# Optimization experiments

Measured on AMD Instinct MI355X. Metric: run time of the kernel, lower is better.

Reference implementation:

```python
import jax, jax.numpy as jnp
import numpy as np
import math

B, T, HID = 2, 2048, 2048
NH, KVH, HD = 16, 4, 128  # num_heads, kv_heads, head_dim


def rotate_half(x):
    x1, x2 = x[..., : x.shape[-1] // 2], x[..., x.shape[-1] // 2 :]
    return jnp.concatenate([-x2, x1], axis=-1)


def setup_inputs() -> dict:
    key = jax.random.key(0)
    ks = jax.random.split(key, 6)
    hidden_states = jax.random.normal(ks[0], (B, T, HID), dtype=jnp.float32)
    # additive causal mask (0 on/below diag, -inf-ish above)
    causal = jnp.triu(jnp.full((T, T), -1e9, dtype=jnp.float32), k=1)
    attention_mask = causal[None, None, :, :]
    # real RoPE angles
    inv_freq = 1.0 / (10000.0 ** (np.arange(0, HD, 2, dtype=np.float32) / HD))
    t = np.arange(T, dtype=np.float32)
    freqs = np.einsum('t,d->td', t, inv_freq)
    emb = np.concatenate([freqs, freqs], axis=-1)  # (T, HD)
    cos = jnp.asarray(np.cos(emb))[None, None, :, :]
    sin = jnp.asarray(np.sin(emb))[None, None, :, :]
    s = 0.02
    Wq = jax.random.normal(ks[1], (HID, NH * HD), dtype=jnp.float32) * s
    Wk = jax.random.normal(ks[2], (HID, KVH * HD), dtype=jnp.float32) * s
    Wv = jax.random.normal(ks[3], (HID, KVH * HD), dtype=jnp.float32) * s
    Wo = jax.random.normal(ks[4], (HID, HID), dtype=jnp.float32) * s
    return dict(hidden_states=hidden_states, attention_mask=attention_mask,
                cos=cos, sin=sin, Wq=Wq, Wk=Wk, Wv=Wv, Wo=Wo)


def reference(hidden_states, attention_mask, cos, sin, Wq, Wk, Wv, Wo):
    b, t, _ = hidden_states.shape
    # projections; weights stored (in, out) so y = x @ W
    q = (hidden_states @ Wq).reshape(b, t, NH, HD).transpose(0, 2, 1, 3)   # (B,H,T,D)
    k = (hidden_states @ Wk).reshape(b, t, KVH, HD).transpose(0, 2, 1, 3)  # (B,Hkv,T,D)
    v = (hidden_states @ Wv).reshape(b, t, KVH, HD).transpose(0, 2, 1, 3)
    # RoPE
    c, s = cos[:, :, :t, :], sin[:, :, :t, :]
    q = q * c + rotate_half(q) * s
    k = k * c + rotate_half(k) * s
    # GQA: repeat_interleave kv heads
    rf = NH // KVH
    k = jnp.repeat(k, rf, axis=1)
    v = jnp.repeat(v, rf, axis=1)
    scores = jnp.einsum('bhtd,bhsd->bhts', q, k) / math.sqrt(HD)
    scores = scores + attention_mask
    probs = jax.nn.softmax(scores.astype(jnp.float32), axis=-1).astype(q.dtype)
    ctx = jnp.einsum('bhts,bhsd->bhtd', probs, v)
    ctx = ctx.transpose(0, 2, 1, 3).reshape(b, t, HID)
    return ctx @ Wo
```

## Files before the change

kernel.cpp:

```cpp
#include <hip/hip_runtime.h>
#include <hip/hip_bf16.h>
#include <math.h>

typedef __bf16 bf16;
typedef __bf16 bf16x4 __attribute__((ext_vector_type(4)));
typedef __bf16 bf16x8 __attribute__((ext_vector_type(8)));
typedef float f32x4 __attribute__((ext_vector_type(4)));

#define B_   2
#define T_   2048
#define HID_ 2048
#define NH_  16
#define KVH_ 4
#define HD_  128

__device__ __forceinline__ void gload_lds16(const bf16* g, bf16* l) {
    __builtin_amdgcn_global_load_lds(
        (const __attribute__((address_space(1))) unsigned int*)g,
        (__attribute__((address_space(3))) unsigned int*)l, 16, 0, 0);
}

__device__ __forceinline__ bf16x8 cat4(bf16x4 a, bf16x4 b) {
    bf16x8 r;
    #pragma unroll
    for (int i = 0; i < 4; i++) { r[i] = a[i]; r[i + 4] = b[i]; }
    return r;
}

__device__ __forceinline__ void transpose_tile(const float* __restrict__ in, bf16* __restrict__ out,
                                               int N, int rowOff, int kt, int nt) {
    __shared__ float tile[32][33];
    int k0 = kt * 32, n0 = nt * 32;
    int tx = threadIdx.x & 31, ty = threadIdx.x >> 5;
    for (int i = ty; i < 32; i += 8)
        tile[i][tx] = in[(size_t)(k0 + i) * N + n0 + tx];
    __syncthreads();
    for (int i = ty; i < 32; i += 8)
        out[(size_t)(rowOff + n0 + i) * 2048 + (k0 + tx)] = (bf16)tile[tx][i];
}

__global__ void prep(const float* __restrict__ hidden, bf16* __restrict__ hid_bf,
                     const float* __restrict__ Wq, const float* __restrict__ Wk,
                     const float* __restrict__ Wv, const float* __restrict__ Wo,
                     bf16* __restrict__ WqkvT, bf16* __restrict__ WoT) {
    int bid = blockIdx.x;
    if (bid < 8192) {
        int i = bid * 256 + threadIdx.x;
        float4 v = ((const float4*)hidden)[i];
        bf16x4 o = { (bf16)v.x, (bf16)v.y, (bf16)v.z, (bf16)v.w };
        ((bf16x4*)hid_bf)[i] = o;
    } else if (bid < 12288) {
        int t = bid - 8192;
        transpose_tile(Wq, WqkvT, 2048, 0, t & 63, t >> 6);
    } else if (bid < 13312) {
        int t = bid - 12288;
        transpose_tile(Wk, WqkvT, 512, 2048, t & 63, t >> 6);
    } else if (bid < 14336) {
        int t = bid - 13312;
        transpose_tile(Wv, WqkvT, 512, 2560, t & 63, t >> 6);
    } else {
        int t = bid - 14336;
        transpose_tile(Wo, WoT, 2048, 0, t & 63, t >> 6);
    }
}


__global__ __launch_bounds__(256, 2) void gemm_qkv_rope(
    const bf16* __restrict__ A, const bf16* __restrict__ BT,
    const float* __restrict__ cosb, const float* __restrict__ sinb,
    bf16* __restrict__ q, bf16* __restrict__ k, bf16* __restrict__ vT) {
    __shared__ __align__(16) char smem[128 * 136 * 2];
    bf16* As = (bf16*)smem;
    bf16* Bs = As + 128 * 32;
    bf16* Cs = (bf16*)smem;
    const int K = 2048;
    int bm = blockIdx.x * 128, hid = blockIdx.y, bn = hid * 128;
    int tid = threadIdx.x, lane = tid & 63, w = tid >> 6;
    int wm = (w & 1) * 64, wn = (w >> 1) * 64;
    int lm = lane & 15, quad = lane >> 4;
    int c0 = w * 64 + lane, c1 = 256 + c0;
    int r0 = c0 >> 2, g0 = (((c0 & 3) ^ ((c0 >> 3) & 3)) * 8);
    int r1 = c1 >> 2, g1 = (((c1 & 3) ^ ((c1 >> 3) & 3)) * 8);
    const bf16* a0 = A  + (size_t)(bm + r0) * K + g0;
    const bf16* a1 = A  + (size_t)(bm + r1) * K + g1;
    const bf16* b0 = BT + (size_t)(bn + r0) * K + g0;
    const bf16* b1 = BT + (size_t)(bn + r1) * K + g1;
    bf16* lA0 = As + (size_t)(w * 64) * 8;
    bf16* lA1 = As + (size_t)(256 + w * 64) * 8;
    bf16* lB0 = Bs + (size_t)(w * 64) * 8;
    bf16* lB1 = Bs + (size_t)(256 + w * 64) * 8;
    int sx = ((quad ^ ((lm >> 1) & 3)) << 3);
    f32x4 acc[4][4] = {};
    for (int k0 = 0; k0 < K; k0 += 32) {
        gload_lds16(a0, lA0); gload_lds16(a1, lA1);
        gload_lds16(b0, lB0); gload_lds16(b1, lB1);
        a0 += 32; a1 += 32; b0 += 32; b1 += 32;
        __syncthreads();
        bf16x8 af[4], bfr[4];
        #pragma unroll
        for (int mt = 0; mt < 4; mt++) af[mt]  = *(const bf16x8*)&As[(wm + mt*16 + lm) * 32 + sx];
        #pragma unroll
        for (int nt = 0; nt < 4; nt++) bfr[nt] = *(const bf16x8*)&Bs[(wn + nt*16 + lm) * 32 + sx];
        #pragma unroll
        for (int mt = 0; mt < 4; mt++)
            #pragma unroll
            for (int nt = 0; nt < 4; nt++)
                acc[mt][nt] = __builtin_amdgcn_mfma_f32_16x16x32_bf16(af[mt], bfr[nt], acc[mt][nt], 0, 0, 0);
        __syncthreads();
    }
    #pragma unroll
    for (int mt = 0; mt < 4; mt++)
        #pragma unroll
        for (int r = 0; r < 4; r++) {
            int row = wm + mt*16 + quad*4 + r;
            #pragma unroll
            for (int nt = 0; nt < 4; nt++)
                Cs[row * 136 + wn + nt*16 + lm] = (bf16)acc[mt][nt][r];
        }
    __syncthreads();

    int b = bm >> 11, t0 = bm & 2047;
    if (hid < 20) {
        bool isq = hid < 16;
        int d = (tid & 15) * 8;
        float sgn = (d < 64) ? -1.f : 1.f;
        float scl = isq ? 0.12752965013239224f : 1.0f;
        bf16* dst = isq ? (q + ((size_t)(b * NH_ + hid) * T_) * HD_)
                        : (k + ((size_t)(b * KVH_ + (hid - 16)) * T_) * HD_);
        #pragma unroll
        for (int i = 0; i < 8; i++) {
            int row = (tid >> 4) + i * 16;
            int t = t0 + row;
            bf16x8 x  = *(const bf16x8*)&Cs[row * 136 + d];
            bf16x8 xo = *(const bf16x8*)&Cs[row * 136 + (d ^ 64)];
            bf16x8 o;
            #pragma unroll
            for (int j = 0; j < 8; j++) {
                float c = cosb[t * 128 + d + j], s = sinb[t * 128 + d + j];
                o[j] = (bf16)(((float)x[j] * c + sgn * (float)xo[j] * s) * scl);
            }
            *(bf16x8*)(dst + (size_t)t * HD_ + d) = o;
        }
    } else {
        int kvh = hid - 20;
        int t6 = (tid & 15) * 4;
        int C = 4 * (t6 >> 5) + ((t6 >> 2) & 3);
        int j0 = 4 * ((t6 >> 4) & 1);
        int pos = 8 * C + j0;
        bf16* dst = vT + (size_t)(b * KVH_ + kvh) * HD_ * T_;
        #pragma unroll
        for (int i = 0; i < 8; i++) {
            int d = (tid >> 4) + i * 16;
            #pragma unroll
            for (int half = 0; half < 2; half++) {
                int tt = half * 64 + t6;
                bf16x4 vv = { Cs[(tt+0)*136 + d], Cs[(tt+1)*136 + d],
                              Cs[(tt+2)*136 + d], Cs[(tt+3)*136 + d] };
                *(bf16x4*)(dst + (size_t)d * T_ + t0 + half * 64 + pos) = vv;
            }
        }
    }
}

__global__ __launch_bounds__(256, 2) void gemm_bf16_nt(
    const bf16* __restrict__ A, const bf16* __restrict__ BT, float* __restrict__ C,
    int M, int N, int K) {
    __shared__ __align__(16) bf16 As[128 * 32];
    __shared__ __align__(16) bf16 Bs[128 * 32];
    int bm = blockIdx.x * 128, bn = blockIdx.y * 128;
    int tid = threadIdx.x, lane = tid & 63, w = tid >> 6;
    int wm = (w & 1) * 64, wn = (w >> 1) * 64;
    int lm = lane & 15, quad = lane >> 4;
    int c0 = w * 64 + lane, c1 = 256 + c0;
    int r0 = c0 >> 2, g0 = (((c0 & 3) ^ ((c0 >> 3) & 3)) * 8);
    int r1 = c1 >> 2, g1 = (((c1 & 3) ^ ((c1 >> 3) & 3)) * 8);
    const bf16* a0 = A  + (size_t)(bm + r0) * K + g0;
    const bf16* a1 = A  + (size_t)(bm + r1) * K + g1;
    const bf16* b0 = BT + (size_t)(bn + r0) * K + g0;
    const bf16* b1 = BT + (size_t)(bn + r1) * K + g1;
    bf16* lA0 = As + (size_t)(w * 64) * 8;
    bf16* lA1 = As + (size_t)(256 + w * 64) * 8;
    bf16* lB0 = Bs + (size_t)(w * 64) * 8;
    bf16* lB1 = Bs + (size_t)(256 + w * 64) * 8;
    int sx = ((quad ^ ((lm >> 1) & 3)) << 3);
    f32x4 acc[4][4] = {};
    for (int k0 = 0; k0 < K; k0 += 32) {
        gload_lds16(a0, lA0); gload_lds16(a1, lA1);
        gload_lds16(b0, lB0); gload_lds16(b1, lB1);
        a0 += 32; a1 += 32; b0 += 32; b1 += 32;
        __syncthreads();
        bf16x8 af[4], bfr[4];
        #pragma unroll
        for (int mt = 0; mt < 4; mt++) af[mt]  = *(const bf16x8*)&As[(wm + mt*16 + lm) * 32 + sx];
        #pragma unroll
        for (int nt = 0; nt < 4; nt++) bfr[nt] = *(const bf16x8*)&Bs[(wn + nt*16 + lm) * 32 + sx];
        #pragma unroll
        for (int mt = 0; mt < 4; mt++)
            #pragma unroll
            for (int nt = 0; nt < 4; nt++)
                acc[mt][nt] = __builtin_amdgcn_mfma_f32_16x16x32_bf16(af[mt], bfr[nt], acc[mt][nt], 0, 0, 0);
        __syncthreads();
    }
    #pragma unroll
    for (int mt = 0; mt < 4; mt++) {
        #pragma unroll
        for (int r = 0; r < 4; r++) {
            int row = bm + wm + mt*16 + quad*4 + r;
            float* cp = C + (size_t)row * N + bn + wn + lm;
            #pragma unroll
            for (int nt = 0; nt < 4; nt++)
                cp[nt*16] = acc[mt][nt][r];
        }
    }
}

__global__ __launch_bounds__(256, 2) void flash_attn(
    const bf16* __restrict__ q, const bf16* __restrict__ k, const bf16* __restrict__ vT,
    bf16* __restrict__ ctx) {
    __shared__ __align__(16) bf16 Ksb[2 * 64 * 128];
    __shared__ __align__(16) bf16 Vpb[2 * 128 * 64];
    int bh = blockIdx.y;
    int b = bh >> 4, h = bh & 15, kvh = h >> 2;
    int tid = threadIdx.x, lane = tid & 63, w = tid >> 6;
    int lm = lane & 15, quad = lane >> 4, kq = quad * 8;
    const bf16* kg = k  + (size_t)(b * KVH_ + kvh) * T_ * HD_;
    const bf16* vg = vT + (size_t)(b * KVH_ + kvh) * HD_ * T_;
    int ksl = lane >> 4;
    int vdl = lane >> 3;
    int vc  = (((lane & 7) ^ (vdl & 7)) << 3);
    int sxv1 = ((quad ^ (lm & 7)) << 3);
    int sxv2 = (((4 + quad) ^ (lm & 7)) << 3);

    auto stage = [&](int s0, int p) {
        bf16* kd = Ksb + p * (64 * 128);
        bf16* vd = Vpb + p * (128 * 64);
        #pragma unroll
        for (int i = 0; i < 4; i++) {
            int srow = w * 16 + i * 4;
            int kc = (((lane & 15) ^ (i * 4 + ksl)) << 3);
            gload_lds16(kg + (size_t)(s0 + srow + ksl) * HD_ + kc, kd + srow * 128);
        }
        #pragma unroll
        for (int i = 0; i < 4; i++) {
            int drow = w * 32 + i * 8;
            gload_lds16(vg + (size_t)(drow + vdl) * T_ + s0 + vc, vd + drow * 64);
        }
    };

    for (int half = 0; half < 2; half++) {
        int qt = (half == 0) ? blockIdx.x : (31 - blockIdx.x);
        const bf16* qg = q + ((size_t)(b * NH_ + h) * T_ + qt*64 + w*16 + lm) * HD_;
        bf16x8 qf[4];
        #pragma unroll
        for (int kk = 0; kk < 4; kk++) qf[kk] = *(const bf16x8*)(qg + kk*32 + kq);

        f32x4 Ot[8] = {};
        float l_ = 0.f;
        int nIter = qt + 1;

        __syncthreads();
        stage(0, 0);

        for (int it = 0; it < nIter; it++) {
            __syncthreads();
            if (it + 1 < nIter) stage((it + 1) * 64, (it + 1) & 1);
            const bf16* ks = Ksb + (it & 1) * (64 * 128);
            const bf16* vp = Vpb + (it & 1) * (128 * 64);

            f32x4 sacc[4] = {};
            #pragma unroll
            for (int n = 0; n < 4; n++)
                #pragma unroll
                for (int kk = 0; kk < 4; kk++) {
                    bf16x8 kf = *(const bf16x8*)&ks[(n*16 + lm) * 128 + (((kk*4 + quad) ^ lm) << 3)];
                    sacc[n] = __builtin_amdgcn_mfma_f32_16x16x32_bf16(kf, qf[kk], sacc[n], 0, 0, 0);
                }
            if (it == qt) {
                #pragma unroll
                for (int n = 0; n < 4; n++)
                    #pragma unroll
                    for (int r = 0; r < 4; r++)
                        if (n*16 + quad*4 + r > w*16 + lm) sacc[n][r] = -1e30f;
            }
            bf16x4 pt[4];
            #pragma unroll
            for (int n = 0; n < 4; n++) {
                f32x4 pe;
                #pragma unroll
                for (int r = 0; r < 4; r++) pe[r] = exp2f(sacc[n][r]);
                l_ += (pe[0] + pe[1]) + (pe[2] + pe[3]);
                #pragma unroll
                for (int r = 0; r < 4; r++) pt[n][r] = (bf16)pe[r];
            }
            bf16x8 pf01 = cat4(pt[0], pt[1]);
            bf16x8 pf23 = cat4(pt[2], pt[3]);
            #pragma unroll
            for (int dt = 0; dt < 8; dt++) {
                const bf16* vr = &vp[(dt*16 + lm) * 64];
                bf16x8 vf01 = *(const bf16x8*)(vr + sxv1);
                Ot[dt] = __builtin_amdgcn_mfma_f32_16x16x32_bf16(vf01, pf01, Ot[dt], 0, 0, 0);
                bf16x8 vf23 = *(const bf16x8*)(vr + sxv2);
                Ot[dt] = __builtin_amdgcn_mfma_f32_16x16x32_bf16(vf23, pf23, Ot[dt], 0, 0, 0);
            }
        }

        l_ += __shfl_xor(l_, 16);
        l_ += __shfl_xor(l_, 32);
        float linv = 1.0f / l_;
        bf16* cp = ctx + ((size_t)(b * T_) + qt*64 + w*16 + lm) * HID_ + h * HD_;
        #pragma unroll
        for (int dt = 0; dt < 8; dt++) {
            bf16x4 o4 = { (bf16)(Ot[dt][0]*linv), (bf16)(Ot[dt][1]*linv),
                          (bf16)(Ot[dt][2]*linv), (bf16)(Ot[dt][3]*linv) };
            *(bf16x4*)(cp + dt*16 + quad*4) = o4;
        }
    }
}

extern "C" void kernel_launch(void* const* d_in, const int* in_sizes, int n_in,
                              void* d_out, int out_size, void* d_ws, size_t ws_size,
                              hipStream_t stream) {
    const float* hidden = (const float*)d_in[0];
    const float* cosb = (const float*)d_in[2];
    const float* sinb = (const float*)d_in[3];
    const float* Wq = (const float*)d_in[4];
    const float* Wk = (const float*)d_in[5];
    const float* Wv = (const float*)d_in[6];
    const float* Wo = (const float*)d_in[7];
    float* out = (float*)d_out;

    char* ws = (char*)d_ws;
    size_t off = 0;
    bf16* hid_bf = (bf16*)(ws + off); off += (size_t)4096*2048*2;
    bf16* WqkvT  = (bf16*)(ws + off); off += (size_t)3072*2048*2;
    bf16* WoT    = (bf16*)(ws + off); off += (size_t)2048*2048*2;
    bf16* qbuf   = (bf16*)(ws + off); off += (size_t)B_*NH_*T_*HD_*2;
    bf16* kbuf   = (bf16*)(ws + off); off += (size_t)B_*KVH_*T_*HD_*2;
    bf16* vtbuf  = (bf16*)(ws + off); off += (size_t)B_*KVH_*HD_*T_*2;
    bf16* ctx    = (bf16*)(ws + off); off += (size_t)4096*2048*2;

    prep<<<18432, 256, 0, stream>>>(hidden, hid_bf, Wq, Wk, Wv, Wo, WqkvT, WoT);
    gemm_qkv_rope<<<dim3(32, 24), 256, 0, stream>>>(hid_bf, WqkvT, cosb, sinb, qbuf, kbuf, vtbuf);
    flash_attn<<<dim3(16, 32), 256, 0, stream>>>(qbuf, kbuf, vtbuf, ctx);
    gemm_bf16_nt<<<dim3(32, 16), 256, 0, stream>>>(ctx, WoT, out, 4096, 2048, 2048);
}
```

Baseline: 299.3 us.

## Rewrite QKV GEMM as 256x256 double-buffered pipelined tile with 8 waves

The QKV projection GEMM moves from 128x128 tiles with a single LDS buffer and BK=32 to 256x256 tiles, 512 threads, BK=64 and a double-buffered LDS ring. Global-to-LDS loads for the next K step are issued between MFMA phases, with s_setprio raised around the MFMA groups, so that memory latency overlaps compute. The RoPE/V-transpose epilogue now processes two heads per block in two passes through a 128-row-stride staging area. The larger tile improves data reuse but uses 128KB of LDS, which limits residency, and leaves only 192 blocks for the GPU's 256 CUs.

```diff
diff --git a/kernel.cpp b/kernel.cpp
--- a/kernel.cpp
+++ b/kernel.cpp
@@ -64,99 +64,189 @@
     }
 }
 
-
-__global__ __launch_bounds__(256, 2) void gemm_qkv_rope(
+__global__ __launch_bounds__(512, 2) void gemm_qkv_rope(
     const bf16* __restrict__ A, const bf16* __restrict__ BT,
     const float* __restrict__ cosb, const float* __restrict__ sinb,
     bf16* __restrict__ q, bf16* __restrict__ k, bf16* __restrict__ vT) {
-    __shared__ __align__(16) char smem[128 * 136 * 2];
-    bf16* As = (bf16*)smem;
-    bf16* Bs = As + 128 * 32;
-    bf16* Cs = (bf16*)smem;
+    __shared__ __align__(16) bf16 smem[2 * 32768];
+    bf16* Cs = smem;
     const int K = 2048;
-    int bm = blockIdx.x * 128, hid = blockIdx.y, bn = hid * 128;
+    int bm = blockIdx.x * 256, by = blockIdx.y, bn = by * 256;
     int tid = threadIdx.x, lane = tid & 63, w = tid >> 6;
-    int wm = (w & 1) * 64, wn = (w >> 1) * 64;
+    int wcol = w & 3;
+    int wm = (w >> 2) * 128, wn = wcol * 64;
     int lm = lane & 15, quad = lane >> 4;
-    int c0 = w * 64 + lane, c1 = 256 + c0;
-    int r0 = c0 >> 2, g0 = (((c0 & 3) ^ ((c0 >> 3) & 3)) * 8);
-    int r1 = c1 >> 2, g1 = (((c1 & 3) ^ ((c1 >> 3) & 3)) * 8);
-    const bf16* a0 = A  + (size_t)(bm + r0) * K + g0;
-    const bf16* a1 = A  + (size_t)(bm + r1) * K + g1;
-    const bf16* b0 = BT + (size_t)(bn + r0) * K + g0;
-    const bf16* b1 = BT + (size_t)(bn + r1) * K + g1;
-    bf16* lA0 = As + (size_t)(w * 64) * 8;
-    bf16* lA1 = As + (size_t)(256 + w * 64) * 8;
-    bf16* lB0 = Bs + (size_t)(w * 64) * 8;
-    bf16* lB1 = Bs + (size_t)(256 + w * 64) * 8;
-    int sx = ((quad ^ ((lm >> 1) & 3)) << 3);
-    f32x4 acc[4][4] = {};
-    for (int k0 = 0; k0 < K; k0 += 32) {
-        gload_lds16(a0, lA0); gload_lds16(a1, lA1);
-        gload_lds16(b0, lB0); gload_lds16(b1, lB1);
-        a0 += 32; a1 += 32; b0 += 32; b1 += 32;
+    int srow = tid >> 3;
+    int scol = ((tid & 7) * 8) ^ ((srow & 7) << 3);
+    const bf16* ga = A  + (size_t)(bm + srow) * K + scol;
+    const bf16* gb = BT + (size_t)(bn + srow) * K + scol;
+    int ldst = w * 512;
+    int fxo = (lm & 7) << 3;
+    f32x4 acc[8][4] = {};
+    bf16x8 af[4][2], b0[2][2], b1[2][2];
+
+#define BARx() do { asm volatile("" ::: "memory");                              \
+                    __builtin_amdgcn_s_barrier();                               \
+                    asm volatile("" ::: "memory"); } while (0)
+
+#define RD_A(MH, CB) do {                                                       \
+        _Pragma("unroll")                                                       \
+        for (int mf = 0; mf < 4; ++mf)                                          \
+            _Pragma("unroll")                                                   \
+            for (int ks = 0; ks < 2; ++ks)                                      \
+                af[mf][ks] = *(const bf16x8*)&(CB)[(wm + (MH)*64 + mf*16 + lm)*64 \
+                                                   + ((ks*32 + quad*8) ^ fxo)]; \
+    } while (0)
+
+#define RD_B(DST, NH, CB) do {                                                  \
+        _Pragma("unroll")                                                       \
+        for (int nf = 0; nf < 2; ++nf)                                          \
+            _Pragma("unroll")                                                   \
+            for (int ks = 0; ks < 2; ++ks)                                      \
+                DST[nf][ks] = *(const bf16x8*)&(CB)[16384                       \
+                                    + (wn + ((NH)*2 + nf)*16 + lm)*64           \
+                                    + ((ks*32 + quad*8) ^ fxo)];                \
+    } while (0)
+
+#define MM(MH, NH, BF) do {                                                     \
+        __builtin_amdgcn_s_setprio(1);                                          \
+        _Pragma("unroll")                                                       \
+        for (int mf = 0; mf < 4; ++mf)                                          \
+            _Pragma("unroll")                                                   \
+            for (int nf = 0; nf < 2; ++nf)                                      \
+                _Pragma("unroll")                                               \
+                for (int ks = 0; ks < 2; ++ks)                                  \
+                    acc[(MH)*4 + mf][(NH)*2 + nf] =                             \
+                        __builtin_amdgcn_mfma_f32_16x16x32_bf16(                \
+                            af[mf][ks], BF[nf][ks],                             \
+                            acc[(MH)*4 + mf][(NH)*2 + nf], 0, 0, 0);            \
+        __builtin_amdgcn_s_setprio(0);                                          \
+    } while (0)
+
+#define STAGE_H(H, NB) do {                                                     \
+        _Pragma("unroll")                                                       \
+        for (int j = 0; j < 2; ++j) {                                           \
+            gload_lds16(ga + 64 + (size_t)((H)*128 + j*64) * K,                 \
+                        (NB) + (H)*8192 + j*4096 + ldst);                       \
+            gload_lds16(gb + 64 + (size_t)((H)*128 + j*64) * K,                 \
+                        (NB) + 16384 + (H)*8192 + j*4096 + ldst);               \
+        }                                                                       \
+    } while (0)
+
+    #pragma unroll
+    for (int h = 0; h < 2; ++h)
+        #pragma unroll
+        for (int j = 0; j < 2; ++j) {
+            gload_lds16(ga + (size_t)(h*128 + j*64) * K, smem + h*8192 + j*4096 + ldst);
+            gload_lds16(gb + (size_t)(h*128 + j*64) * K, smem + 16384 + h*8192 + j*4096 + ldst);
+        }
+    asm volatile("s_waitcnt vmcnt(0)" ::: "memory");
+    BARx();
+
+    for (int t = 0; t < 31; ++t) {
+        bf16* cb = smem + (t & 1) * 32768;
+        bf16* nb = smem + ((t + 1) & 1) * 32768;
+        RD_A(0, cb);
+        RD_B(b0, 0, cb);
+        STAGE_H(0, nb);
+        BARx();
+        MM(0, 0, b0);
+        asm volatile("s_waitcnt vmcnt(4)" ::: "memory");
+        BARx();
+        RD_B(b1, 1, cb);
+        STAGE_H(1, nb);
+        BARx();
+        MM(0, 1, b1);
+        BARx();
+        RD_A(1, cb);
+        BARx();
+        MM(1, 1, b1);
+        BARx();
+        MM(1, 0, b0);
+        asm volatile("s_waitcnt vmcnt(4)" ::: "memory");
+        BARx();
+        ga += 64; gb += 64;
+    }
+    {
+        bf16* cb = smem + 32768;
+        RD_A(0, cb);
+        RD_B(b0, 0, cb);
+        BARx();
+        MM(0, 0, b0);
+        asm volatile("s_waitcnt vmcnt(0)" ::: "memory");
+        BARx();
+        RD_B(b1, 1, cb);
+        BARx();
+        MM(0, 1, b1);
+        BARx();
+        RD_A(1, cb);
+        BARx();
+        MM(1, 1, b1);
+        BARx();
+        MM(1, 0, b0);
+        BARx();
+    }
+#undef BARx
+#undef RD_A
+#undef RD_B
+#undef MM
+#undef STAGE_H
+
+    int b = bm >> 11, t0 = bm & 2047;
+    for (int hh = 0; hh < 2; ++hh) {
         __syncthreads();
-        bf16x8 af[4], bfr[4];
-        #pragma unroll
-        for (int mt = 0; mt < 4; mt++) af[mt]  = *(const bf16x8*)&As[(wm + mt*16 + lm) * 32 + sx];
-        #pragma unroll
-        for (int nt = 0; nt < 4; nt++) bfr[nt] = *(const bf16x8*)&Bs[(wn + nt*16 + lm) * 32 + sx];
-        #pragma unroll
-        for (int mt = 0; mt < 4; mt++)
-            #pragma unroll
-            for (int nt = 0; nt < 4; nt++)
-                acc[mt][nt] = __builtin_amdgcn_mfma_f32_16x16x32_bf16(af[mt], bfr[nt], acc[mt][nt], 0, 0, 0);
+        if ((wcol >> 1) == hh) {
+            #pragma unroll
+            for (int mfg = 0; mfg < 8; ++mfg)
+                #pragma unroll
+                for (int r = 0; r < 4; ++r) {
+                    int row = wm + (mfg >> 2) * 64 + (mfg & 3) * 16 + quad * 4 + r;
+                    #pragma unroll
+                    for (int nfg = 0; nfg < 4; ++nfg)
+                        Cs[row * 136 + (wcol & 1) * 64 + nfg * 16 + lm] = (bf16)acc[mfg][nfg][r];
+                }
+        }
         __syncthreads();
-    }
-    #pragma unroll
-    for (int mt = 0; mt < 4; mt++)
-        #pragma unroll
-        for (int r = 0; r < 4; r++) {
-            int row = wm + mt*16 + quad*4 + r;
-            #pragma unroll
-            for (int nt = 0; nt < 4; nt++)
-                Cs[row * 136 + wn + nt*16 + lm] = (bf16)acc[mt][nt][r];
-        }
-    __syncthreads();
-
-    int b = bm >> 11, t0 = bm & 2047;
-    if (hid < 20) {
-        bool isq = hid < 16;
-        int d = (tid & 15) * 8;
-        float sgn = (d < 64) ? -1.f : 1.f;
-        float scl = isq ? 0.12752965013239224f : 1.0f;
-        bf16* dst = isq ? (q + ((size_t)(b * NH_ + hid) * T_) * HD_)
-                        : (k + ((size_t)(b * KVH_ + (hid - 16)) * T_) * HD_);
-        #pragma unroll
-        for (int i = 0; i < 8; i++) {
-            int row = (tid >> 4) + i * 16;
-            int t = t0 + row;
-            bf16x8 x  = *(const bf16x8*)&Cs[row * 136 + d];
-            bf16x8 xo = *(const bf16x8*)&Cs[row * 136 + (d ^ 64)];
-            bf16x8 o;
-            #pragma unroll
-            for (int j = 0; j < 8; j++) {
-                float c = cosb[t * 128 + d + j], s = sinb[t * 128 + d + j];
-                o[j] = (bf16)(((float)x[j] * c + sgn * (float)xo[j] * s) * scl);
+        if (by < 10) {
+            bool isq = by < 8;
+            int hd = isq ? (by * 2 + hh) : ((by - 8) * 2 + hh);
+            int d = (tid & 15) * 8;
+            float sgn = (d < 64) ? -1.f : 1.f;
+            float scl = isq ? 0.12752965013239224f : 1.0f;
+            bf16* dst = isq ? (q + ((size_t)(b * NH_ + hd) * T_) * HD_)
+                            : (k + ((size_t)(b * KVH_ + hd) * T_) * HD_);
+            #pragma unroll
+            for (int i = 0; i < 8; ++i) {
+                int row = (tid >> 4) + i * 32;
+                int t = t0 + row;
+                bf16x8 x  = *(const bf16x8*)&Cs[row * 136 + d];
+                bf16x8 xo = *(const bf16x8*)&Cs[row * 136 + (d ^ 64)];
+                bf16x8 o;
+                #pragma unroll
+                for (int j = 0; j < 8; ++j) {
+                    float c = cosb[t * 128 + d + j], s = sinb[t * 128 + d + j];
+                    o[j] = (bf16)(((float)x[j] * c + sgn * (float)xo[j] * s) * scl);
+                }
+                *(bf16x8*)(dst + (size_t)t * HD_ + d) = o;
             }
-            *(bf16x8*)(dst + (size_t)t * HD_ + d) = o;
-        }
-    } else {
-        int kvh = hid - 20;
-        int t6 = (tid & 15) * 4;
-        int C = 4 * (t6 >> 5) + ((t6 >> 2) & 3);
-        int j0 = 4 * ((t6 >> 4) & 1);
-        int pos = 8 * C + j0;
-        bf16* dst = vT + (size_t)(b * KVH_ + kvh) * HD_ * T_;
-        #pragma unroll
-        for (int i = 0; i < 8; i++) {
-            int d = (tid >> 4) + i * 16;
-            #pragma unroll
-            for (int half = 0; half < 2; half++) {
-                int tt = half * 64 + t6;
-                bf16x4 vv = { Cs[(tt+0)*136 + d], Cs[(tt+1)*136 + d],
-                              Cs[(tt+2)*136 + d], Cs[(tt+3)*136 + d] };
-                *(bf16x4*)(dst + (size_t)d * T_ + t0 + half * 64 + pos) = vv;
+        } else {
+            int kvh = (by - 10) * 2 + hh;
+            int tb = tid >> 8, tl = tid & 255;
+            int t6 = (tl & 15) * 4;
+            int Cc = 4 * (t6 >> 5) + ((t6 >> 2) & 3);
+            int j0 = 4 * ((t6 >> 4) & 1);
+            int pos = 8 * Cc + j0;
+            bf16* dst = vT + (size_t)(b * KVH_ + kvh) * HD_ * T_;
+            #pragma unroll
+            for (int i = 0; i < 8; ++i) {
+                int d = (tl >> 4) + i * 16;
+                #pragma unroll
+                for (int hv = 0; hv < 2; ++hv) {
+                    int rr = tb * 128 + hv * 64 + t6;
+                    bf16x4 vv = { Cs[(rr + 0) * 136 + d], Cs[(rr + 1) * 136 + d],
+                                  Cs[(rr + 2) * 136 + d], Cs[(rr + 3) * 136 + d] };
+                    *(bf16x4*)(dst + (size_t)d * T_ + t0 + tb * 128 + hv * 64 + pos) = vv;
+                }
             }
         }
     }
@@ -340,7 +430,7 @@
     bf16* ctx    = (bf16*)(ws + off); off += (size_t)4096*2048*2;
 
     prep<<<18432, 256, 0, stream>>>(hidden, hid_bf, Wq, Wk, Wv, Wo, WqkvT, WoT);
-    gemm_qkv_rope<<<dim3(32, 24), 256, 0, stream>>>(hid_bf, WqkvT, cosb, sinb, qbuf, kbuf, vtbuf);
+    gemm_qkv_rope<<<dim3(16, 12), 512, 0, stream>>>(hid_bf, WqkvT, cosb, sinb, qbuf, kbuf, vtbuf);
     flash_attn<<<dim3(16, 32), 256, 0, stream>>>(qbuf, kbuf, vtbuf, ctx);
     gemm_bf16_nt<<<dim3(32, 16), 256, 0, stream>>>(ctx, WoT, out, 4096, 2048, 2048);
 }
```

New measurement: 306.7 us. +2.5%, slower.
